# Optimization experiments

Measured on AMD Instinct MI355X. Metric: run time of the kernel, lower is better.

## Reference

```python
import jax, jax.numpy as jnp
import numpy as np

N, E, H, C, HID, B = 50000, 1600000, 2, 64, 256, 1024
HC = H * C  # 128


def setup_inputs() -> dict:
    key = jax.random.key(0)
    ks = jax.random.split(key, 12)
    s = 1.0 / np.sqrt(HC)
    return {
        "x": jax.random.normal(ks[0], (N, 1), jnp.float32),
        "edge_index": jax.random.randint(ks[1], (2, E), 0, N, jnp.int64),
        "edge_attr": jax.random.normal(ks[2], (E, 1), jnp.float32),
        "message": jax.random.normal(ks[3], (B, HID), jnp.float32),
        # GATv2Conv params (in_channels=1, out=C per head, heads=H, edge_dim=1)
        "W_l": jax.random.normal(ks[4], (1, HC), jnp.float32) * s,
        "b_l": jnp.zeros((HC,), jnp.float32),
        "W_r": jax.random.normal(ks[5], (1, HC), jnp.float32) * s,
        "b_r": jnp.zeros((HC,), jnp.float32),
        "W_e": jax.random.normal(ks[6], (1, HC), jnp.float32) * s,
        "att": jax.random.normal(ks[7], (H, C), jnp.float32) * s,
        "bias_out": jnp.zeros((HC,), jnp.float32),
        # fc: Linear(hidden_size, 2*embedding_size)
        "fc_W": jax.random.normal(ks[8], (HC, HID), jnp.float32) / np.sqrt(HID),
        "fc_b": jnp.zeros((HC,), jnp.float32),
    }


def gatv2(x, edge_index, edge_attr, W_l, b_l, W_r, b_r, W_e, att, bias_out):
    n = x.shape[0]
    src, dst = edge_index[0], edge_index[1]
    xl = (x @ W_l + b_l).reshape(n, H, C)  # source transform
    xr = (x @ W_r + b_r).reshape(n, H, C)  # target transform
    e = (edge_attr @ W_e).reshape(-1, H, C)
    # per-edge message: [E, H, C]
    m = jax.nn.leaky_relu(xl[src] + xr[dst] + e, 0.2)
    logits = jnp.einsum('ehc,hc->eh', m, att)  # [E, H]
    # segment softmax over incoming edges of each dst node
    lmax = jax.ops.segment_max(logits, dst, num_segments=n)
    lmax = jnp.where(jnp.isfinite(lmax), lmax, 0.0)
    ex = jnp.exp(logits - lmax[dst])
    denom = jax.ops.segment_sum(ex, dst, num_segments=n)
    alpha = ex / (denom[dst] + 1e-16)  # [E, H]
    out = jax.ops.segment_sum(alpha[:, :, None] * xl[src], dst, num_segments=n)
    return out.reshape(n, HC) + bias_out


def reference(x, edge_index, edge_attr, message, W_l, b_l, W_r, b_r, W_e, att, bias_out, fc_W, fc_b):
    g = gatv2(x, edge_index, edge_attr, W_l, b_l, W_r, b_r, W_e, att, bias_out)  # [N, 2*emb]
    me = message @ fc_W.T + fc_b  # [B, 2*emb]
    dots = g @ me.T  # [N, B]
    return jax.nn.softmax(dots, axis=1)
```

## Files before the change

### kernel.cpp

```cpp
#include <hip/hip_runtime.h>
#include <hip/hip_bf16.h>

#define NHEAD 2
#define CDIM  64
#define HC    128
#define HID   256
#define BCOLS 1024
#define CHUNK 2048
#define BSH   7
#define BNODES 128
#define MAXBUCK 512
#define EB    8

#define KOFF 8.0f

__global__ __launch_bounds__(256) void count_kernel(
    const int* __restrict__ ei, unsigned* __restrict__ counts,
    int E, int nblk, int nbuck)
{
    __shared__ unsigned hist[MAXBUCK];
    int t = threadIdx.x, b = blockIdx.x;
    for (int i = t; i < nbuck; i += 256) hist[i] = 0;
    __syncthreads();
    int start = b * CHUNK;
    #pragma unroll
    for (int u = 0; u < CHUNK / 256; ++u) {
        int e = start + u * 256 + t;
        if (e < E) atomicAdd(&hist[((unsigned)ei[E + e]) >> BSH], 1u);
    }
    __syncthreads();
    for (int i = t; i < nbuck; i += 256) counts[(size_t)i * nblk + b] = hist[i];
}

__global__ __launch_bounds__(64) void scan_bucket_kernel(
    const unsigned* __restrict__ counts, unsigned* __restrict__ off,
    unsigned* __restrict__ totals, int nblk)
{
    int bk = blockIdx.x, ln = threadIdx.x;
    const unsigned* c = counts + (size_t)bk * nblk;
    unsigned* o = off + (size_t)bk * nblk;
    unsigned running = 0;
    for (int b0 = 0; b0 < nblk; b0 += 64) {
        int i = b0 + ln;
        unsigned v = (i < nblk) ? c[i] : 0u;
        unsigned s = v;
        #pragma unroll
        for (int d = 1; d < 64; d <<= 1) {
            unsigned p = __shfl_up(s, d);
            if (ln >= d) s += p;
        }
        if (i < nblk) o[i] = running + s - v;
        running += __shfl(s, 63);
    }
    if (ln == 0) totals[bk] = running;
}

__global__ __launch_bounds__(64) void scan_base_kernel(
    const unsigned* __restrict__ totals, unsigned* __restrict__ base, int nbuck)
{
    int ln = threadIdx.x;
    unsigned running = 0;
    for (int b0 = 0; b0 < nbuck; b0 += 64) {
        int i = b0 + ln;
        unsigned v = (i < nbuck) ? totals[i] : 0u;
        unsigned s = v;
        #pragma unroll
        for (int d = 1; d < 64; d <<= 1) {
            unsigned p = __shfl_up(s, d);
            if (ln >= d) s += p;
        }
        if (i < nbuck) base[i] = running + s - v;
        running += __shfl(s, 63);
    }
}

__global__ __launch_bounds__(256) void scatter_perm_kernel(
    const int* __restrict__ ei,
    const unsigned* __restrict__ off, const unsigned* __restrict__ base,
    unsigned* __restrict__ perm, int E, int nblk, int nbuck)
{
    __shared__ unsigned cursor[MAXBUCK];
    int t = threadIdx.x, b = blockIdx.x;
    for (int i = t; i < nbuck; i += 256)
        cursor[i] = base[i] + off[(size_t)i * nblk + b];
    __syncthreads();
    int start = b * CHUNK;
    #pragma unroll
    for (int u = 0; u < CHUNK / 256; ++u) {
        int e = start + u * 256 + t;
        if (e < E) {
            unsigned bk = ((unsigned)ei[E + e]) >> BSH;
            unsigned pos = atomicAdd(&cursor[bk], 1u);
            perm[pos] = (unsigned)e;
        }
    }
}

__global__ __launch_bounds__(256, 4) void accum_kernel(
    const float* __restrict__ x, const int* __restrict__ ei,
    const float* __restrict__ ea,
    const float* __restrict__ Wl, const float* __restrict__ bl,
    const float* __restrict__ Wr, const float* __restrict__ br,
    const float* __restrict__ We, const float* __restrict__ att,
    const unsigned* __restrict__ perm,
    const unsigned* __restrict__ base, const unsigned* __restrict__ totals,
    unsigned long long* __restrict__ accP,
    int E, int N)
{
    __shared__ float swl[HC], swr[HC], swe[HC], sat[HC], sbs[HC];
    __shared__ unsigned acc4[BNODES][4];
    int t = threadIdx.x;
    int bk = blockIdx.x >> 1;
    int s  = blockIdx.x & 1;
    if (t < HC) {
        swl[t] = Wl[t]; swr[t] = Wr[t]; swe[t] = We[t];
        sat[t] = att[t]; sbs[t] = bl[t] + br[t];
    }
    if (t < BNODES) { acc4[t][0] = 0; acc4[t][1] = 0; acc4[t][2] = 0; acc4[t][3] = 0; }
    __syncthreads();

    unsigned b0 = base[bk], tot = totals[bk];
    unsigned lo = b0 + (tot * (unsigned)s) / 2u;
    unsigned hi = b0 + (tot * (unsigned)(s + 1)) / 2u;

    for (unsigned ib = lo + t; ib < hi; ib += 256u * EB) {
        unsigned pk[EB];
        int sk[EB], dk[EB];
        float ak[EB], xs[EB], xd[EB];
        #pragma unroll
        for (int k = 0; k < EB; ++k) {
            unsigned i = ib + (unsigned)k * 256u;
            pk[k] = (i < hi) ? perm[i] : 0xffffffffu;
        }
        #pragma unroll
        for (int k = 0; k < EB; ++k) {
            if (pk[k] != 0xffffffffu) {
                sk[k] = ei[pk[k]]; dk[k] = ei[E + pk[k]]; ak[k] = ea[pk[k]];
            } else { sk[k] = 0; dk[k] = 0; ak[k] = 0.f; }
        }
        #pragma unroll
        for (int k = 0; k < EB; ++k) { xs[k] = x[sk[k]]; xd[k] = x[dk[k]]; }

        float l0[EB], l1[EB];
        #pragma unroll
        for (int k = 0; k < EB; ++k) { l0[k] = 0.f; l1[k] = 0.f; }

        #pragma unroll 2
        for (int c = 0; c < CDIM; ++c) {
            float wl0 = swl[c],      wr0 = swr[c],      we0 = swe[c];
            float bs0 = sbs[c],      at0 = sat[c];
            float wl1 = swl[c + 64], wr1 = swr[c + 64], we1 = swe[c + 64];
            float bs1 = sbs[c + 64], at1 = sat[c + 64];
            #pragma unroll
            for (int k = 0; k < EB; ++k) {
                float v0 = fmaf(xs[k], wl0, fmaf(xd[k], wr0, fmaf(ak[k], we0, bs0)));
                v0 = fmaxf(v0, 0.2f * v0);
                l0[k] = fmaf(v0, at0, l0[k]);
                float v1 = fmaf(xs[k], wl1, fmaf(xd[k], wr1, fmaf(ak[k], we1, bs1)));
                v1 = fmaxf(v1, 0.2f * v1);
                l1[k] = fmaf(v1, at1, l1[k]);
            }
        }

        #pragma unroll
        for (int k = 0; k < EB; ++k) {
            if (pk[k] == 0xffffffffu) continue;
            float ex0 = __expf(l0[k]), ex1 = __expf(l1[k]);
            float w = xs[k] + KOFF;
            int d = dk[k] & (BNODES - 1);
            atomicAdd(&acc4[d][0], (unsigned)(ex0 * 65536.0f + 0.5f));
            atomicAdd(&acc4[d][1], (unsigned)(ex0 * w * 1048576.0f + 0.5f));
            atomicAdd(&acc4[d][2], (unsigned)(ex1 * 65536.0f + 0.5f));
            atomicAdd(&acc4[d][3], (unsigned)(ex1 * w * 1048576.0f + 0.5f));
        }
    }
    __syncthreads();

    int nl = t >> 1, h = t & 1;
    int node = bk * BNODES + nl;
    if (node < N) {
        unsigned long long v =
            ((unsigned long long)acc4[nl][2 * h] << 32) | acc4[nl][2 * h + 1];
        if (v) atomicAdd(&accP[node * 2 + h], v);
    }
}

__global__ __launch_bounds__(128) void me_y_kernel(
    const float* __restrict__ message, const float* __restrict__ fcW,
    const float* __restrict__ fcb,
    const float* __restrict__ Wl, const float* __restrict__ bl,
    const float* __restrict__ bias_out,
    float* __restrict__ y)
{
    __shared__ float msg[HID];
    __shared__ float part[3][2];
    int b = blockIdx.x, t = threadIdx.x;
    msg[t]       = message[b * HID + t];
    msg[t + 128] = message[b * HID + 128 + t];
    __syncthreads();
    float acc = fcb[t];
    const float4* w4 = (const float4*)(fcW + t * HID);
    const float4* m4 = (const float4*)msg;
    #pragma unroll
    for (int q = 0; q < HID / 4; ++q) {
        float4 w = w4[q], m = m4[q];
        acc = fmaf(w.x, m.x, fmaf(w.y, m.y, fmaf(w.z, m.z, fmaf(w.w, m.w, acc))));
    }
    float p0 = Wl[t] * acc, p1 = bl[t] * acc, p2 = bias_out[t] * acc;
    #pragma unroll
    for (int d = 1; d < 64; d <<= 1) {
        p0 += __shfl_xor(p0, d); p1 += __shfl_xor(p1, d); p2 += __shfl_xor(p2, d);
    }
    int wv = t >> 6;
    if ((t & 63) == 0) { part[0][wv] = p0; part[1][wv] = p1; part[2][wv] = p2; }
    __syncthreads();
    if (t == 0) {
        y[0 * BCOLS + b] = part[0][0];
        y[1 * BCOLS + b] = part[0][1];
        y[2 * BCOLS + b] = part[1][0];
        y[3 * BCOLS + b] = part[1][1];
        y[4 * BCOLS + b] = part[2][0] + part[2][1];
    }
}

__global__ __launch_bounds__(256) void row_softmax_kernel(
    const unsigned long long* __restrict__ accP,
    const float* __restrict__ y,
    float* __restrict__ out, int N)
{
    __shared__ float ys[5][BCOLS];
    int t = threadIdx.x;
    for (int r = t; r < 5 * BCOLS; r += 256)
        ((float*)ys)[r] = y[r];
    __syncthreads();

    int wv = t >> 6, ln = t & 63;
    int node = blockIdx.x * 4 + wv;
    if (node >= N) return;

    unsigned long long v0 = accP[node * 2 + 0];
    unsigned long long v1 = accP[node * 2 + 1];
    float S0 = 0.f, T0 = 0.f, S1 = 0.f, T1 = 0.f;
    if (v0 != 0ULL) {
        double den  = (double)(v0 >> 32) * (1.0 / 65536.0);
        double nump = (double)(v0 & 0xffffffffULL) * (1.0 / 1048576.0);
        S0 = (float)((nump - (double)KOFF * den) / den);
        T0 = (float)(den / (den + 1e-16));
    }
    if (v1 != 0ULL) {
        double den  = (double)(v1 >> 32) * (1.0 / 65536.0);
        double nump = (double)(v1 & 0xffffffffULL) * (1.0 / 1048576.0);
        S1 = (float)((nump - (double)KOFF * den) / den);
        T1 = (float)(den / (den + 1e-16));
    }

    float e[16];
    float sum = 0.f;
    #pragma unroll
    for (int u = 0; u < 4; ++u) {
        int c = ln * 4 + u * 256;
        float4 a  = *(const float4*)&ys[0][c];
        float4 b2 = *(const float4*)&ys[1][c];
        float4 c2 = *(const float4*)&ys[2][c];
        float4 d2 = *(const float4*)&ys[3][c];
        float4 k2 = *(const float4*)&ys[4][c];
        float lx = fmaf(S0, a.x, fmaf(S1, b2.x, fmaf(T0, c2.x, fmaf(T1, d2.x, k2.x))));
        float ly = fmaf(S0, a.y, fmaf(S1, b2.y, fmaf(T0, c2.y, fmaf(T1, d2.y, k2.y))));
        float lz = fmaf(S0, a.z, fmaf(S1, b2.z, fmaf(T0, c2.z, fmaf(T1, d2.z, k2.z))));
        float lw = fmaf(S0, a.w, fmaf(S1, b2.w, fmaf(T0, c2.w, fmaf(T1, d2.w, k2.w))));
        e[u * 4 + 0] = __expf(lx); e[u * 4 + 1] = __expf(ly);
        e[u * 4 + 2] = __expf(lz); e[u * 4 + 3] = __expf(lw);
        sum += e[u * 4 + 0] + e[u * 4 + 1] + e[u * 4 + 2] + e[u * 4 + 3];
    }
    #pragma unroll
    for (int d = 1; d < 64; d <<= 1) sum += __shfl_xor(sum, d);
    float inv = 1.f / sum;

    float* orow = out + (size_t)node * BCOLS;
    #pragma unroll
    for (int u = 0; u < 4; ++u) {
        float4 o = make_float4(e[u * 4 + 0] * inv, e[u * 4 + 1] * inv,
                               e[u * 4 + 2] * inv, e[u * 4 + 3] * inv);
        *(float4*)(orow + ln * 4 + u * 256) = o;
    }
}

extern "C" void kernel_launch(void* const* d_in, const int* in_sizes, int n_in,
                              void* d_out, int out_size, void* d_ws, size_t ws_size,
                              hipStream_t stream) {
    const float* x        = (const float*)d_in[0];
    const int*   ei       = (const int*)d_in[1];
    const float* ea       = (const float*)d_in[2];
    const float* message  = (const float*)d_in[3];
    const float* Wl       = (const float*)d_in[4];
    const float* bl       = (const float*)d_in[5];
    const float* Wr       = (const float*)d_in[6];
    const float* br       = (const float*)d_in[7];
    const float* We       = (const float*)d_in[8];
    const float* att      = (const float*)d_in[9];
    const float* bias_out = (const float*)d_in[10];
    const float* fcW      = (const float*)d_in[11];
    const float* fcb      = (const float*)d_in[12];

    int N = in_sizes[0];
    int E = in_sizes[2];
    int B = in_sizes[3] / HID;
    int n2 = N * 2;
    int nblk  = (E + CHUNK - 1) / CHUNK;
    int nbuck = (N + BNODES - 1) / BNODES;

    unsigned long long* accP = (unsigned long long*)d_ws;
    float* y = (float*)(accP + (size_t)n2);

    char* ob = (char*)d_out;
    unsigned* perm   = (unsigned*)ob;
    unsigned* counts = (unsigned*)(ob + (size_t)E * 4);
    unsigned* off    = counts + (size_t)nbuck * nblk;
    unsigned* totals = off + (size_t)nbuck * nblk;
    unsigned* basep  = totals + nbuck;

    hipMemsetAsync(accP, 0, sizeof(unsigned long long) * (size_t)n2, stream);
    me_y_kernel<<<B, 128, 0, stream>>>(message, fcW, fcb, Wl, bl, bias_out, y);
    count_kernel<<<nblk, 256, 0, stream>>>(ei, counts, E, nblk, nbuck);
    scan_bucket_kernel<<<nbuck, 64, 0, stream>>>(counts, off, totals, nblk);
    scan_base_kernel<<<1, 64, 0, stream>>>(totals, basep, nbuck);
    scatter_perm_kernel<<<nblk, 256, 0, stream>>>(ei, off, basep, perm, E, nblk, nbuck);
    accum_kernel<<<nbuck * 2, 256, 0, stream>>>(x, ei, ea, Wl, bl, Wr, br, We, att,
                                                perm, basep, totals, accP, E, N);
    row_softmax_kernel<<<(N + 3) / 4, 256, 0, stream>>>(accP, y, (float*)d_out, N);
}
```

Before: 173.4 us.

## Scatter packed edge payload instead of permutation indices, stage dst x in LDS

The bucket scatter now writes a packed 64-bit payload per edge (edge_attr bits, 16-bit src index, 7-bit local dst) instead of just the edge id. This removes the dependent gather of edge_index and edge_attr through the permutation in the accumulation kernel. Destination x values are read from a per-bucket LDS cache rather than from global memory. The separate memset of the accumulator is folded into count_kernel. In exchange, the scatter writes twice as many bytes, the payload buffer is larger, and packing src into 16 bits only holds when N <= 65536.

```diff
diff --git a/kernel.cpp b/kernel.cpp
--- a/kernel.cpp
+++ b/kernel.cpp
@@ -14,13 +14,17 @@
 
 #define KOFF 8.0f
 
+
 __global__ __launch_bounds__(256) void count_kernel(
     const int* __restrict__ ei, unsigned* __restrict__ counts,
+    unsigned long long* __restrict__ accP, int n2,
     int E, int nblk, int nbuck)
 {
     __shared__ unsigned hist[MAXBUCK];
     int t = threadIdx.x, b = blockIdx.x;
     for (int i = t; i < nbuck; i += 256) hist[i] = 0;
+    int zi = b * 128 + t;
+    if (t < 128 && zi < n2) accP[zi] = 0ULL;
     __syncthreads();
     int start = b * CHUNK;
     #pragma unroll
@@ -74,10 +78,10 @@
     }
 }
 
-__global__ __launch_bounds__(256) void scatter_perm_kernel(
-    const int* __restrict__ ei,
+__global__ __launch_bounds__(256) void scatter_pay_kernel(
+    const int* __restrict__ ei, const float* __restrict__ ea,
     const unsigned* __restrict__ off, const unsigned* __restrict__ base,
-    unsigned* __restrict__ perm, int E, int nblk, int nbuck)
+    unsigned long long* __restrict__ pay, int E, int nblk, int nbuck)
 {
     __shared__ unsigned cursor[MAXBUCK];
     int t = threadIdx.x, b = blockIdx.x;
@@ -89,26 +93,30 @@
     for (int u = 0; u < CHUNK / 256; ++u) {
         int e = start + u * 256 + t;
         if (e < E) {
-            unsigned bk = ((unsigned)ei[E + e]) >> BSH;
+            unsigned src = (unsigned)ei[e];
+            unsigned dst = (unsigned)ei[E + e];
+            unsigned ab  = __float_as_uint(ea[e]);
+            unsigned bk  = dst >> BSH;
             unsigned pos = atomicAdd(&cursor[bk], 1u);
-            perm[pos] = (unsigned)e;
+            pay[pos] = ((unsigned long long)ab << 32) |
+                       ((unsigned long long)src << 7) | (dst & 127u);
         }
     }
 }
 
 __global__ __launch_bounds__(256, 4) void accum_kernel(
-    const float* __restrict__ x, const int* __restrict__ ei,
-    const float* __restrict__ ea,
+    const float* __restrict__ x,
     const float* __restrict__ Wl, const float* __restrict__ bl,
     const float* __restrict__ Wr, const float* __restrict__ br,
     const float* __restrict__ We, const float* __restrict__ att,
-    const unsigned* __restrict__ perm,
+    const unsigned long long* __restrict__ pay,
     const unsigned* __restrict__ base, const unsigned* __restrict__ totals,
     unsigned long long* __restrict__ accP,
-    int E, int N)
+    int N)
 {
     __shared__ float swl[HC], swr[HC], swe[HC], sat[HC], sbs[HC];
-    __shared__ unsigned acc4[BNODES][4];
+    __shared__ float xds[BNODES];
+    __shared__ unsigned acc5[BNODES][5];
     int t = threadIdx.x;
     int bk = blockIdx.x >> 1;
     int s  = blockIdx.x & 1;
@@ -116,7 +124,11 @@
         swl[t] = Wl[t]; swr[t] = Wr[t]; swe[t] = We[t];
         sat[t] = att[t]; sbs[t] = bl[t] + br[t];
     }
-    if (t < BNODES) { acc4[t][0] = 0; acc4[t][1] = 0; acc4[t][2] = 0; acc4[t][3] = 0; }
+    if (t < BNODES) {
+        int node = bk * BNODES + t;
+        xds[t] = (node < N) ? x[node] : 0.f;
+    }
+    for (int i = t; i < BNODES * 5; i += 256) ((unsigned*)acc5)[i] = 0;
     __syncthreads();
 
     unsigned b0 = base[bk], tot = totals[bk];
@@ -124,22 +136,26 @@
     unsigned hi = b0 + (tot * (unsigned)(s + 1)) / 2u;
 
     for (unsigned ib = lo + t; ib < hi; ib += 256u * EB) {
-        unsigned pk[EB];
-        int sk[EB], dk[EB];
-        float ak[EB], xs[EB], xd[EB];
+        unsigned vm = 0;
+        unsigned long long pk[EB];
         #pragma unroll
         for (int k = 0; k < EB; ++k) {
             unsigned i = ib + (unsigned)k * 256u;
-            pk[k] = (i < hi) ? perm[i] : 0xffffffffu;
-        }
+            if (i < hi) { pk[k] = pay[i]; vm |= (1u << k); }
+            else          pk[k] = 0ULL;
+        }
+        int   d7[EB];
+        float ak[EB], xs[EB], xd[EB];
         #pragma unroll
         for (int k = 0; k < EB; ++k) {
-            if (pk[k] != 0xffffffffu) {
-                sk[k] = ei[pk[k]]; dk[k] = ei[E + pk[k]]; ak[k] = ea[pk[k]];
-            } else { sk[k] = 0; dk[k] = 0; ak[k] = 0.f; }
-        }
-        #pragma unroll
-        for (int k = 0; k < EB; ++k) { xs[k] = x[sk[k]]; xd[k] = x[dk[k]]; }
+            d7[k] = (int)(pk[k] & 127u);
+            ak[k] = __uint_as_float((unsigned)(pk[k] >> 32));
+        }
+        #pragma unroll
+        for (int k = 0; k < EB; ++k)
+            xs[k] = x[(unsigned)(pk[k] >> 7) & 0xFFFFu];
+        #pragma unroll
+        for (int k = 0; k < EB; ++k) xd[k] = xds[d7[k]];
 
         float l0[EB], l1[EB];
         #pragma unroll
@@ -164,14 +180,14 @@
 
         #pragma unroll
         for (int k = 0; k < EB; ++k) {
-            if (pk[k] == 0xffffffffu) continue;
+            if (!(vm & (1u << k))) continue;
             float ex0 = __expf(l0[k]), ex1 = __expf(l1[k]);
             float w = xs[k] + KOFF;
-            int d = dk[k] & (BNODES - 1);
-            atomicAdd(&acc4[d][0], (unsigned)(ex0 * 65536.0f + 0.5f));
-            atomicAdd(&acc4[d][1], (unsigned)(ex0 * w * 1048576.0f + 0.5f));
-            atomicAdd(&acc4[d][2], (unsigned)(ex1 * 65536.0f + 0.5f));
-            atomicAdd(&acc4[d][3], (unsigned)(ex1 * w * 1048576.0f + 0.5f));
+            int d = d7[k];
+            atomicAdd(&acc5[d][0], (unsigned)(ex0 * 65536.0f + 0.5f));
+            atomicAdd(&acc5[d][1], (unsigned)(ex0 * w * 1048576.0f + 0.5f));
+            atomicAdd(&acc5[d][2], (unsigned)(ex1 * 65536.0f + 0.5f));
+            atomicAdd(&acc5[d][3], (unsigned)(ex1 * w * 1048576.0f + 0.5f));
         }
     }
     __syncthreads();
@@ -180,7 +196,7 @@
     int node = bk * BNODES + nl;
     if (node < N) {
         unsigned long long v =
-            ((unsigned long long)acc4[nl][2 * h] << 32) | acc4[nl][2 * h + 1];
+            ((unsigned long long)acc5[nl][2 * h] << 32) | acc5[nl][2 * h + 1];
         if (v) atomicAdd(&accP[node * 2 + h], v);
     }
 }
@@ -313,19 +329,18 @@
     float* y = (float*)(accP + (size_t)n2);
 
     char* ob = (char*)d_out;
-    unsigned* perm   = (unsigned*)ob;
-    unsigned* counts = (unsigned*)(ob + (size_t)E * 4);
+    unsigned long long* pay = (unsigned long long*)ob;
+    unsigned* counts = (unsigned*)(ob + (size_t)E * 8);
     unsigned* off    = counts + (size_t)nbuck * nblk;
     unsigned* totals = off + (size_t)nbuck * nblk;
     unsigned* basep  = totals + nbuck;
 
-    hipMemsetAsync(accP, 0, sizeof(unsigned long long) * (size_t)n2, stream);
     me_y_kernel<<<B, 128, 0, stream>>>(message, fcW, fcb, Wl, bl, bias_out, y);
-    count_kernel<<<nblk, 256, 0, stream>>>(ei, counts, E, nblk, nbuck);
+    count_kernel<<<nblk, 256, 0, stream>>>(ei, counts, accP, n2, E, nblk, nbuck);
     scan_bucket_kernel<<<nbuck, 64, 0, stream>>>(counts, off, totals, nblk);
     scan_base_kernel<<<1, 64, 0, stream>>>(totals, basep, nbuck);
-    scatter_perm_kernel<<<nblk, 256, 0, stream>>>(ei, off, basep, perm, E, nblk, nbuck);
-    accum_kernel<<<nbuck * 2, 256, 0, stream>>>(x, ei, ea, Wl, bl, Wr, br, We, att,
-                                                perm, basep, totals, accP, E, N);
+    scatter_pay_kernel<<<nblk, 256, 0, stream>>>(ei, ea, off, basep, pay, E, nblk, nbuck);
+    accum_kernel<<<nbuck * 2, 256, 0, stream>>>(x, Wl, bl, Wr, br, We, att,
+                                                pay, basep, totals, accP, N);
     row_softmax_kernel<<<(N + 3) / 4, 256, 0, stream>>>(accP, y, (float*)d_out, N);
 }
```

Result: faster. 151.0 us (-12.9%).
